# Performance work log

Measured on AMD Instinct MI355X. Metric: run time of the kernel, lower is better.

## Reference

```python
import jax, jax.numpy as jnp
import numpy as np

EMBED = 128
HEADS = 8
HEAD_DIM = EMBED // HEADS


def setup_inputs() -> dict:
    key = jax.random.key(0)
    ks = jax.random.split(key, 11)
    B, T, N, C = 8, 64, 170, EMBED
    s = 1.0 / np.sqrt(C)
    return {
        "values": jax.random.normal(ks[0], (B, T, N, C), dtype=jnp.float32),
        "keys": jax.random.normal(ks[1], (B, T, N, C), dtype=jnp.float32),
        "query": jax.random.normal(ks[2], (B, T, N, C), dtype=jnp.float32),
        "Wv": jax.random.normal(ks[3], (C, C), dtype=jnp.float32) * s,
        "bv": jnp.zeros((C,), dtype=jnp.float32),
        "Wk": jax.random.normal(ks[4], (C, C), dtype=jnp.float32) * s,
        "bk": jnp.zeros((C,), dtype=jnp.float32),
        "Wq": jax.random.normal(ks[5], (C, C), dtype=jnp.float32) * s,
        "bq": jnp.zeros((C,), dtype=jnp.float32),
        "Wo": jax.random.normal(ks[6], (C, C), dtype=jnp.float32) * s,
        "bo": jnp.zeros((C,), dtype=jnp.float32),
    }


def reference(values, keys, query, Wv, bv, Wk, bk, Wq, bq, Wo, bo):
    B, T, N, C = query.shape
    H, D = HEADS, HEAD_DIM
    # Linear projections (torch nn.Linear: x @ W.T + b)
    v = (values @ Wv.T + bv).reshape(B, T, N, H, D)
    k = (keys @ Wk.T + bk).reshape(B, T, N, H, D)
    q = (query @ Wq.T + bq).reshape(B, T, N, H, D)
    # spatial mode: attention over nodes N, independent per (b, t, h)
    energy = jnp.einsum('btqhd,btkhd->btqkh', q, k)  # [B,T,N,N,H]
    scale = jnp.asarray(C, q.dtype) ** 0.5
    attn = jax.nn.softmax(energy / scale, axis=3)
    out = jnp.einsum('btqkh,btkhd->btqhd', attn, v).reshape(B, T, N, H * D)
    return out @ Wo.T + bo
```

## Files before the change

kernel.cpp:

```cpp
#include <hip/hip_runtime.h>
#include <cstdint>

typedef float   f32x4  __attribute__((ext_vector_type(4)));
typedef __bf16  bf16x4 __attribute__((ext_vector_type(4)));
typedef __bf16  bf16x8 __attribute__((ext_vector_type(8)));

#if __has_builtin(__builtin_amdgcn_exp2f)
#define EXP2F(x) __builtin_amdgcn_exp2f(x)
#else
#define EXP2F(x) exp2f(x)
#endif

#define BT_TOTAL 512
#define NNODES 170
#define CDIM 128
#define HEADS 8
#define HDIM 16
#define SLAB (NNODES*HDIM)
#define NPAD 172
#define VSLAB (HDIM*NPAD)
#define QKV_ELEMS ((size_t)BT_TOTAL*HEADS*SLAB)
#define S2L2E 0.12753851f

__global__ __launch_bounds__(512) void qkv_kernel(const float* __restrict__ qin,
    const float* __restrict__ kin, const float* __restrict__ vin,
    const float* __restrict__ Wq, const float* __restrict__ Wk, const float* __restrict__ Wv,
    const float* __restrict__ bq, const float* __restrict__ bk, const float* __restrict__ bv,
    __bf16* __restrict__ qws, __bf16* __restrict__ kws, __bf16* __restrict__ vt) {
    __shared__ __bf16 Wl[128 * 132];
    int t = threadIdx.x;
    int iid = blockIdx.x / BT_TOTAL;
    int bt  = blockIdx.x % BT_TOTAL;
    const float* X    = (iid == 0) ? qin : (iid == 1) ? kin : vin;
    const float* W    = (iid == 0) ? Wq  : (iid == 1) ? Wk  : Wv;
    const float* bias = (iid == 0) ? bq  : (iid == 1) ? bk  : bv;
    float wscale = (iid == 0) ? S2L2E : 1.0f;
    #pragma unroll
    for (int i = 0; i < 8; ++i) {
        int idx = i * 512 + t;
        int r = idx >> 5, c = (idx & 31) * 4;
        f32x4 w4 = *(const f32x4*)&W[r * 128 + c];
        bf16x4 wb = { (__bf16)(w4[0] * wscale), (__bf16)(w4[1] * wscale),
                      (__bf16)(w4[2] * wscale), (__bf16)(w4[3] * wscale) };
        *(bf16x4*)&Wl[r * 132 + c] = wb;
    }
    __syncthreads();

    int w = t >> 6, lane = t & 63, li = lane & 15, l4 = lane >> 4;
    f32x4 zf = {0.f, 0.f, 0.f, 0.f};
    for (int mt = 0; mt < 2; ++mt) {
        int tbase = mt * 128 + w * 16;
        if (tbase >= NNODES) break;
        int mrow = tbase + li;
        bool mvalid = mrow < NNODES;
        const float* xrow = X + ((size_t)(bt * NNODES + mrow)) * CDIM;
        f32x4 acc[8] = {};
        #pragma unroll
        for (int kk = 0; kk < 4; ++kk) {
            int kb = kk * 32 + l4 * 4;
            f32x4 a0 = mvalid ? *(const f32x4*)(xrow + kb)      : zf;
            f32x4 a1 = mvalid ? *(const f32x4*)(xrow + kb + 16) : zf;
            bf16x8 a = { (__bf16)a0[0], (__bf16)a0[1], (__bf16)a0[2], (__bf16)a0[3],
                         (__bf16)a1[0], (__bf16)a1[1], (__bf16)a1[2], (__bf16)a1[3] };
            if (iid < 2) {
                #pragma unroll
                for (int nt = 0; nt < 8; ++nt) {
                    int c = nt * 16 + li;
                    bf16x4 b0 = *(const bf16x4*)&Wl[c * 132 + kb];
                    bf16x4 b1 = *(const bf16x4*)&Wl[c * 132 + kb + 16];
                    bf16x8 b = __builtin_shufflevector(b0, b1, 0, 1, 2, 3, 4, 5, 6, 7);
                    acc[nt] = __builtin_amdgcn_mfma_f32_16x16x32_bf16(b, a, acc[nt], 0, 0, 0);
                }
            } else {
                #pragma unroll
                for (int nt = 0; nt < 8; ++nt) {
                    int c = nt * 16 + li;
                    bf16x4 b0 = *(const bf16x4*)&Wl[c * 132 + kb];
                    bf16x4 b1 = *(const bf16x4*)&Wl[c * 132 + kb + 16];
                    bf16x8 b = __builtin_shufflevector(b0, b1, 0, 1, 2, 3, 4, 5, 6, 7);
                    acc[nt] = __builtin_amdgcn_mfma_f32_16x16x32_bf16(a, b, acc[nt], 0, 0, 0);
                }
            }
        }
        if (iid < 2) {
            __bf16* outb = ((iid == 0) ? qws : kws) + ((size_t)bt * HEADS) * SLAB;
            int n = tbase + li;
            if (n < NNODES) {
                #pragma unroll
                for (int nt = 0; nt < 8; ++nt) {
                    f32x4 b4 = *(const f32x4*)&bias[nt * 16 + l4 * 4];
                    f32x4 o = acc[nt] + b4 * wscale;
                    bf16x4 o4 = { (__bf16)o[0], (__bf16)o[1], (__bf16)o[2], (__bf16)o[3] };
                    *(bf16x4*)&outb[(size_t)nt * SLAB + n * HDIM + l4 * 4] = o4;
                }
            }
        } else {
            __bf16* outb = vt + ((size_t)bt * HEADS) * VSLAB;
            int n0 = tbase + l4 * 4;
            #pragma unroll
            for (int nt = 0; nt < 8; ++nt) {
                int c = nt * 16 + li;
                float bval = bias[c];
                __bf16* dst = outb + (size_t)nt * VSLAB + li * NPAD + n0;
                if (n0 + 3 < NNODES) {
                    bf16x4 o4 = { (__bf16)(acc[nt][0] + bval), (__bf16)(acc[nt][1] + bval),
                                  (__bf16)(acc[nt][2] + bval), (__bf16)(acc[nt][3] + bval) };
                    *(bf16x4*)dst = o4;
                } else {
                    #pragma unroll
                    for (int r = 0; r < 4; ++r)
                        if (n0 + r < NNODES) dst[r] = (__bf16)(acc[nt][r] + bval);
                }
            }
        }
    }
}

__global__ __launch_bounds__(256) void attn_kernel(const __bf16* __restrict__ qws,
                                                   const __bf16* __restrict__ kws,
                                                   const __bf16* __restrict__ vt,
                                                   __bf16* __restrict__ ows) {
    int unit = blockIdx.x * 4 + (threadIdx.x >> 6);
    int half = unit & 1, bh = unit >> 1;
    int bt = bh >> 3, h = bh & 7;
    int lane = threadIdx.x & 63, li = lane & 15, l4 = lane >> 4;
    const __bf16* qb  = qws + ((size_t)(bt * HEADS + h)) * SLAB;
    const __bf16* kb  = kws + ((size_t)(bt * HEADS + h)) * SLAB;
    const __bf16* vtb = vt  + ((size_t)(bt * HEADS + h)) * VSLAB;
    __bf16* ob = ows + (size_t)bt * NNODES * CDIM + h * HDIM;
    const __bf16 bz = (__bf16)0.0f;
    const bf16x4 z4 = {bz, bz, bz, bz};
    const f32x4 zf = {0.f, 0.f, 0.f, 0.f};

    bf16x4 kf[11];
    #pragma unroll
    for (int tt = 0; tt < 11; ++tt)
        kf[tt] = *(const bf16x4*)&kb[(tt * 16 + li) * HDIM + l4 * 4];

    bf16x8 vf[6];
    #pragma unroll
    for (int s = 0; s < 5; ++s) {
        bf16x4 a = *(const bf16x4*)&vtb[li * NPAD + 32 * s + 4 * l4];
        bf16x4 b = *(const bf16x4*)&vtb[li * NPAD + 32 * s + 4 * l4 + 16];
        vf[s] = __builtin_shufflevector(a, b, 0, 1, 2, 3, 4, 5, 6, 7);
    }
    {
        bf16x4 a = *(const bf16x4*)&vtb[li * NPAD + 160 + 4 * l4];
        bf16x8 v5 = { (160 + 4 * l4 + 0 < NNODES) ? a[0] : bz,
                      (160 + 4 * l4 + 1 < NNODES) ? a[1] : bz,
                      (160 + 4 * l4 + 2 < NNODES) ? a[2] : bz,
                      (160 + 4 * l4 + 3 < NNODES) ? a[3] : bz,
                      bz, bz, bz, bz };
        vf[5] = v5;
    }
    f32x4 mk = { (160 + l4 * 4 + 0 < NNODES) ? 1.f : 0.f,
                 (160 + l4 * 4 + 1 < NNODES) ? 1.f : 0.f,
                 (160 + l4 * 4 + 2 < NNODES) ? 1.f : 0.f,
                 (160 + l4 * 4 + 3 < NNODES) ? 1.f : 0.f };

    int q0 = half ? 6 : 0;
    int qn = half ? 5 : 6;
    for (int qi = 0; qi < qn; ++qi) {
        int qc = q0 + qi;
        bf16x4 qv = *(const bf16x4*)&qb[(qc * 16 + li) * HDIM + l4 * 4];
        bf16x8 qf = __builtin_shufflevector(qv, z4, 0, 1, 2, 3, 4, 5, 6, 7);
        bf16x4 ph[11];
        f32x4 s4 = zf;
        #pragma unroll
        for (int tt = 0; tt < 11; ++tt) {
            bf16x8 a = __builtin_shufflevector(kf[tt], z4, 0, 1, 2, 3, 4, 5, 6, 7);
            f32x4 e = __builtin_amdgcn_mfma_f32_16x16x32_bf16(a, qf, zf, 0, 0, 0);
            f32x4 p;
            p[0] = EXP2F(e[0]); p[1] = EXP2F(e[1]);
            p[2] = EXP2F(e[2]); p[3] = EXP2F(e[3]);
            if (tt == 10) p *= mk;
            s4 += p;
            ph[tt] = __builtin_convertvector(p, bf16x4);
        }
        float sum = (s4[0] + s4[1]) + (s4[2] + s4[3]);
        sum += __shfl_xor(sum, 16);
        sum += __shfl_xor(sum, 32);
        float inv = 1.0f / sum;
        f32x4 o0 = zf, o1 = zf;
        o0 = __builtin_amdgcn_mfma_f32_16x16x32_bf16(vf[0],
                __builtin_shufflevector(ph[0], ph[1], 0,1,2,3,4,5,6,7), o0, 0,0,0);
        o1 = __builtin_amdgcn_mfma_f32_16x16x32_bf16(vf[1],
                __builtin_shufflevector(ph[2], ph[3], 0,1,2,3,4,5,6,7), o1, 0,0,0);
        o0 = __builtin_amdgcn_mfma_f32_16x16x32_bf16(vf[2],
                __builtin_shufflevector(ph[4], ph[5], 0,1,2,3,4,5,6,7), o0, 0,0,0);
        o1 = __builtin_amdgcn_mfma_f32_16x16x32_bf16(vf[3],
                __builtin_shufflevector(ph[6], ph[7], 0,1,2,3,4,5,6,7), o1, 0,0,0);
        o0 = __builtin_amdgcn_mfma_f32_16x16x32_bf16(vf[4],
                __builtin_shufflevector(ph[8], ph[9], 0,1,2,3,4,5,6,7), o0, 0,0,0);
        o1 = __builtin_amdgcn_mfma_f32_16x16x32_bf16(vf[5],
                __builtin_shufflevector(ph[10], z4,    0,1,2,3,4,5,6,7), o1, 0,0,0);
        f32x4 o = o0 + o1;
        int q = qc * 16 + li;
        if (q < NNODES) {
            bf16x4 ov = { (__bf16)(o[0] * inv), (__bf16)(o[1] * inv),
                          (__bf16)(o[2] * inv), (__bf16)(o[3] * inv) };
            *(bf16x4*)&ob[(size_t)q * CDIM + l4 * 4] = ov;
        }
    }
}

__global__ __launch_bounds__(512) void oproj_kernel(const __bf16* __restrict__ ows,
                                                    const float* __restrict__ Wo,
                                                    const float* __restrict__ bo,
                                                    float* __restrict__ out) {
    __shared__ __bf16 Wl[128 * 132];
    int t = threadIdx.x;
    int bt = blockIdx.x;
    #pragma unroll
    for (int i = 0; i < 8; ++i) {
        int idx = i * 512 + t;
        int r = idx >> 5, c = (idx & 31) * 4;
        f32x4 w4 = *(const f32x4*)&Wo[r * 128 + c];
        bf16x4 wb = { (__bf16)w4[0], (__bf16)w4[1], (__bf16)w4[2], (__bf16)w4[3] };
        *(bf16x4*)&Wl[r * 132 + c] = wb;
    }
    __syncthreads();

    int w = t >> 6, lane = t & 63, li = lane & 15, l4 = lane >> 4;
    const bf16x4 z4 = {(__bf16)0.f, (__bf16)0.f, (__bf16)0.f, (__bf16)0.f};
    for (int mt = 0; mt < 2; ++mt) {
        int tbase = mt * 128 + w * 16;
        if (tbase >= NNODES) break;
        int mrow = tbase + li;
        bool mvalid = mrow < NNODES;
        const __bf16* arow = ows + ((size_t)bt * NNODES + mrow) * CDIM;
        f32x4 acc[8] = {};
        #pragma unroll
        for (int kk = 0; kk < 4; ++kk) {
            int kb = kk * 32 + l4 * 4;
            bf16x4 a0 = mvalid ? *(const bf16x4*)(arow + kb)      : z4;
            bf16x4 a1 = mvalid ? *(const bf16x4*)(arow + kb + 16) : z4;
            bf16x8 a = __builtin_shufflevector(a0, a1, 0, 1, 2, 3, 4, 5, 6, 7);
            #pragma unroll
            for (int nt = 0; nt < 8; ++nt) {
                int c = nt * 16 + li;
                bf16x4 b0 = *(const bf16x4*)&Wl[c * 132 + kb];
                bf16x4 b1 = *(const bf16x4*)&Wl[c * 132 + kb + 16];
                bf16x8 b = __builtin_shufflevector(b0, b1, 0, 1, 2, 3, 4, 5, 6, 7);
                acc[nt] = __builtin_amdgcn_mfma_f32_16x16x32_bf16(b, a, acc[nt], 0, 0, 0);
            }
        }
        int n = tbase + li;
        if (n < NNODES) {
            float* orow = out + ((size_t)bt * NNODES + n) * CDIM;
            #pragma unroll
            for (int nt = 0; nt < 8; ++nt) {
                f32x4 b4 = *(const f32x4*)&bo[nt * 16 + l4 * 4];
                f32x4 o = acc[nt] + b4;
                *(f32x4*)&orow[nt * 16 + l4 * 4] = o;
            }
        }
    }
}

extern "C" void kernel_launch(void* const* d_in, const int* in_sizes, int n_in,
                              void* d_out, int out_size, void* d_ws, size_t ws_size,
                              hipStream_t stream) {
    const float* values = (const float*)d_in[0];
    const float* keys   = (const float*)d_in[1];
    const float* query  = (const float*)d_in[2];
    const float* Wv = (const float*)d_in[3];
    const float* bv = (const float*)d_in[4];
    const float* Wk = (const float*)d_in[5];
    const float* bk = (const float*)d_in[6];
    const float* Wq = (const float*)d_in[7];
    const float* bq = (const float*)d_in[8];
    const float* Wo = (const float*)d_in[9];
    const float* bo = (const float*)d_in[10];
    float* out = (float*)d_out;

    __bf16* qws = (__bf16*)d_ws;
    __bf16* kws = qws + QKV_ELEMS;
    __bf16* ows = kws + QKV_ELEMS;
    __bf16* vt  = (__bf16*)d_out;

    hipLaunchKernelGGL(qkv_kernel,  dim3(1536), dim3(512), 0, stream,
                       query, keys, values, Wq, Wk, Wv, bq, bk, bv, qws, kws, vt);
    hipLaunchKernelGGL(attn_kernel, dim3(2048), dim3(256), 0, stream, qws, kws, vt, ows);
    hipLaunchKernelGGL(oproj_kernel, dim3(512), dim3(512), 0, stream, ows, Wo, bo, out);
}
```

Baseline: 102.2 us.

## Fuse QKV projection, attention and output projection into one per-timestep kernel

Merges the three kernels into one block per (b,t). The block computes Q, K and V into shared memory, runs attention for all 8 heads (one wave per head), stages the head outputs in shared memory and applies the output projection there. A small pre-kernel converts all four weight matrices to bf16 in MFMA fragment order so waves can load them straight into registers. This removes the global round-trips for Q/K/V/O intermediates and two launches. In exchange it uses 128KB of shared memory per block, so only 512 blocks run at low occupancy, and each wave holds 32 weight fragments in registers.

```diff
diff --git a/kernel.cpp b/kernel.cpp
--- a/kernel.cpp
+++ b/kernel.cpp
@@ -16,243 +16,227 @@
 #define CDIM 128
 #define HEADS 8
 #define HDIM 16
-#define SLAB (NNODES*HDIM)
 #define NPAD 172
-#define VSLAB (HDIM*NPAD)
-#define QKV_ELEMS ((size_t)BT_TOTAL*HEADS*SLAB)
 #define S2L2E 0.12753851f
 
-__global__ __launch_bounds__(512) void qkv_kernel(const float* __restrict__ qin,
+#define QOFF 0
+#define KOFF 21760
+#define VOFF 43520
+#define OSTRIDE 132
+#define SMEM_ELEMS 65536
+
+__global__ __launch_bounds__(256) void wconv_kernel(const float* __restrict__ wq,
+                                                    const float* __restrict__ wk,
+                                                    const float* __restrict__ wv,
+                                                    const float* __restrict__ wo,
+                                                    __bf16* __restrict__ wbf) {
+    int idx = blockIdx.x * 256 + threadIdx.x;
+    if (idx >= 4 * 16384) return;
+    int mat = idx >> 14, rem = idx & 16383;
+    int c = rem >> 7, o = rem & 127;
+    int kk = o >> 5, l4 = (o & 31) >> 3, j = o & 7;
+    int col = kk * 32 + l4 * 4 + (j & 3) + 16 * (j >> 2);
+    const float* W = (mat == 0) ? wq : (mat == 1) ? wk : (mat == 2) ? wv : wo;
+    float scale = (mat == 0) ? S2L2E : 1.0f;
+    wbf[idx] = (__bf16)(W[c * 128 + col] * scale);
+}
+
+__global__ __launch_bounds__(512, 2) void fused_kernel(const float* __restrict__ qin,
     const float* __restrict__ kin, const float* __restrict__ vin,
-    const float* __restrict__ Wq, const float* __restrict__ Wk, const float* __restrict__ Wv,
-    const float* __restrict__ bq, const float* __restrict__ bk, const float* __restrict__ bv,
-    __bf16* __restrict__ qws, __bf16* __restrict__ kws, __bf16* __restrict__ vt) {
-    __shared__ __bf16 Wl[128 * 132];
-    int t = threadIdx.x;
-    int iid = blockIdx.x / BT_TOTAL;
-    int bt  = blockIdx.x % BT_TOTAL;
-    const float* X    = (iid == 0) ? qin : (iid == 1) ? kin : vin;
-    const float* W    = (iid == 0) ? Wq  : (iid == 1) ? Wk  : Wv;
-    const float* bias = (iid == 0) ? bq  : (iid == 1) ? bk  : bv;
-    float wscale = (iid == 0) ? S2L2E : 1.0f;
-    #pragma unroll
-    for (int i = 0; i < 8; ++i) {
-        int idx = i * 512 + t;
-        int r = idx >> 5, c = (idx & 31) * 4;
-        f32x4 w4 = *(const f32x4*)&W[r * 128 + c];
-        bf16x4 wb = { (__bf16)(w4[0] * wscale), (__bf16)(w4[1] * wscale),
-                      (__bf16)(w4[2] * wscale), (__bf16)(w4[3] * wscale) };
-        *(bf16x4*)&Wl[r * 132 + c] = wb;
-    }
-    __syncthreads();
-
-    int w = t >> 6, lane = t & 63, li = lane & 15, l4 = lane >> 4;
-    f32x4 zf = {0.f, 0.f, 0.f, 0.f};
-    for (int mt = 0; mt < 2; ++mt) {
-        int tbase = mt * 128 + w * 16;
-        if (tbase >= NNODES) break;
-        int mrow = tbase + li;
-        bool mvalid = mrow < NNODES;
-        const float* xrow = X + ((size_t)(bt * NNODES + mrow)) * CDIM;
-        f32x4 acc[8] = {};
-        #pragma unroll
-        for (int kk = 0; kk < 4; ++kk) {
-            int kb = kk * 32 + l4 * 4;
-            f32x4 a0 = mvalid ? *(const f32x4*)(xrow + kb)      : zf;
-            f32x4 a1 = mvalid ? *(const f32x4*)(xrow + kb + 16) : zf;
-            bf16x8 a = { (__bf16)a0[0], (__bf16)a0[1], (__bf16)a0[2], (__bf16)a0[3],
-                         (__bf16)a1[0], (__bf16)a1[1], (__bf16)a1[2], (__bf16)a1[3] };
-            if (iid < 2) {
-                #pragma unroll
-                for (int nt = 0; nt < 8; ++nt) {
-                    int c = nt * 16 + li;
-                    bf16x4 b0 = *(const bf16x4*)&Wl[c * 132 + kb];
-                    bf16x4 b1 = *(const bf16x4*)&Wl[c * 132 + kb + 16];
-                    bf16x8 b = __builtin_shufflevector(b0, b1, 0, 1, 2, 3, 4, 5, 6, 7);
-                    acc[nt] = __builtin_amdgcn_mfma_f32_16x16x32_bf16(b, a, acc[nt], 0, 0, 0);
-                }
-            } else {
-                #pragma unroll
-                for (int nt = 0; nt < 8; ++nt) {
-                    int c = nt * 16 + li;
-                    bf16x4 b0 = *(const bf16x4*)&Wl[c * 132 + kb];
-                    bf16x4 b1 = *(const bf16x4*)&Wl[c * 132 + kb + 16];
-                    bf16x8 b = __builtin_shufflevector(b0, b1, 0, 1, 2, 3, 4, 5, 6, 7);
-                    acc[nt] = __builtin_amdgcn_mfma_f32_16x16x32_bf16(a, b, acc[nt], 0, 0, 0);
-                }
-            }
-        }
-        if (iid < 2) {
-            __bf16* outb = ((iid == 0) ? qws : kws) + ((size_t)bt * HEADS) * SLAB;
-            int n = tbase + li;
-            if (n < NNODES) {
-                #pragma unroll
-                for (int nt = 0; nt < 8; ++nt) {
-                    f32x4 b4 = *(const f32x4*)&bias[nt * 16 + l4 * 4];
-                    f32x4 o = acc[nt] + b4 * wscale;
-                    bf16x4 o4 = { (__bf16)o[0], (__bf16)o[1], (__bf16)o[2], (__bf16)o[3] };
-                    *(bf16x4*)&outb[(size_t)nt * SLAB + n * HDIM + l4 * 4] = o4;
-                }
-            }
-        } else {
-            __bf16* outb = vt + ((size_t)bt * HEADS) * VSLAB;
-            int n0 = tbase + l4 * 4;
-            #pragma unroll
-            for (int nt = 0; nt < 8; ++nt) {
-                int c = nt * 16 + li;
-                float bval = bias[c];
-                __bf16* dst = outb + (size_t)nt * VSLAB + li * NPAD + n0;
-                if (n0 + 3 < NNODES) {
-                    bf16x4 o4 = { (__bf16)(acc[nt][0] + bval), (__bf16)(acc[nt][1] + bval),
-                                  (__bf16)(acc[nt][2] + bval), (__bf16)(acc[nt][3] + bval) };
-                    *(bf16x4*)dst = o4;
-                } else {
-                    #pragma unroll
-                    for (int r = 0; r < 4; ++r)
-                        if (n0 + r < NNODES) dst[r] = (__bf16)(acc[nt][r] + bval);
-                }
-            }
-        }
-    }
-}
-
-__global__ __launch_bounds__(256) void attn_kernel(const __bf16* __restrict__ qws,
-                                                   const __bf16* __restrict__ kws,
-                                                   const __bf16* __restrict__ vt,
-                                                   __bf16* __restrict__ ows) {
-    int unit = blockIdx.x * 4 + (threadIdx.x >> 6);
-    int half = unit & 1, bh = unit >> 1;
-    int bt = bh >> 3, h = bh & 7;
-    int lane = threadIdx.x & 63, li = lane & 15, l4 = lane >> 4;
-    const __bf16* qb  = qws + ((size_t)(bt * HEADS + h)) * SLAB;
-    const __bf16* kb  = kws + ((size_t)(bt * HEADS + h)) * SLAB;
-    const __bf16* vtb = vt  + ((size_t)(bt * HEADS + h)) * VSLAB;
-    __bf16* ob = ows + (size_t)bt * NNODES * CDIM + h * HDIM;
+    const __bf16* __restrict__ wbf,
+    const float* __restrict__ bq, const float* __restrict__ bk,
+    const float* __restrict__ bv, const float* __restrict__ bo,
+    float* __restrict__ out) {
+    __shared__ __align__(16) __bf16 smem[SMEM_ELEMS];
+    __bf16* qL = smem + QOFF;
+    __bf16* kL = smem + KOFF;
+    __bf16* vL = smem + VOFF;
+    __bf16* oL = smem;
+
+    int bt = blockIdx.x;
+    int t = threadIdx.x, w = t >> 6, lane = t & 63, li = lane & 15, l4 = lane >> 4;
     const __bf16 bz = (__bf16)0.0f;
     const bf16x4 z4 = {bz, bz, bz, bz};
     const f32x4 zf = {0.f, 0.f, 0.f, 0.f};
 
-    bf16x4 kf[11];
+    {
+        int iid = (w < 3) ? 0 : (w < 6 ? 1 : 2);
+        int g   = w - ((iid == 0) ? 0 : (iid == 1) ? 3 : 6);
+        int nw  = (iid == 2) ? 2 : 3;
+        const float* X    = (iid == 0) ? qin : (iid == 1) ? kin : vin;
+        const float* bias = (iid == 0) ? bq  : (iid == 1) ? bk  : bv;
+        float wscale = (iid == 0) ? S2L2E : 1.0f;
+        const __bf16* wb = wbf + iid * 16384;
+        bf16x8 bf[8][4];
+        #pragma unroll
+        for (int nt = 0; nt < 8; ++nt)
+            #pragma unroll
+            for (int kk = 0; kk < 4; ++kk)
+                bf[nt][kk] = *(const bf16x8*)&wb[(nt * 16 + li) * 128 + kk * 32 + l4 * 8];
+
+        for (int tile = g; tile < 11; tile += nw) {
+            int tbase = tile * 16;
+            int mrow = tbase + li;
+            bool mvalid = mrow < NNODES;
+            const float* xrow = X + ((size_t)(bt * NNODES + mrow)) * CDIM;
+            f32x4 acc[8] = {};
+            #pragma unroll
+            for (int kk = 0; kk < 4; ++kk) {
+                int kb = kk * 32 + l4 * 4;
+                f32x4 a0 = mvalid ? *(const f32x4*)(xrow + kb)      : zf;
+                f32x4 a1 = mvalid ? *(const f32x4*)(xrow + kb + 16) : zf;
+                bf16x8 a = { (__bf16)a0[0], (__bf16)a0[1], (__bf16)a0[2], (__bf16)a0[3],
+                             (__bf16)a1[0], (__bf16)a1[1], (__bf16)a1[2], (__bf16)a1[3] };
+                if (iid < 2) {
+                    #pragma unroll
+                    for (int nt = 0; nt < 8; ++nt)
+                        acc[nt] = __builtin_amdgcn_mfma_f32_16x16x32_bf16(bf[nt][kk], a, acc[nt], 0, 0, 0);
+                } else {
+                    #pragma unroll
+                    for (int nt = 0; nt < 8; ++nt)
+                        acc[nt] = __builtin_amdgcn_mfma_f32_16x16x32_bf16(a, bf[nt][kk], acc[nt], 0, 0, 0);
+                }
+            }
+            if (iid < 2) {
+                __bf16* dst = (iid == 0) ? qL : kL;
+                int n = tbase + li;
+                if (n < NNODES) {
+                    #pragma unroll
+                    for (int nt = 0; nt < 8; ++nt) {
+                        f32x4 b4 = *(const f32x4*)&bias[nt * 16 + l4 * 4];
+                        f32x4 ov = acc[nt] + b4 * wscale;
+                        bf16x4 o4 = { (__bf16)ov[0], (__bf16)ov[1], (__bf16)ov[2], (__bf16)ov[3] };
+                        *(bf16x4*)&dst[nt * (NNODES * HDIM) + n * HDIM + l4 * 4] = o4;
+                    }
+                }
+            } else {
+                int n0 = tbase + l4 * 4;
+                #pragma unroll
+                for (int nt = 0; nt < 8; ++nt) {
+                    float bval = bias[nt * 16 + li];
+                    __bf16* d2 = vL + nt * (HDIM * NPAD) + li * NPAD + n0;
+                    if (n0 + 3 < NNODES) {
+                        bf16x4 o4 = { (__bf16)(acc[nt][0] + bval), (__bf16)(acc[nt][1] + bval),
+                                      (__bf16)(acc[nt][2] + bval), (__bf16)(acc[nt][3] + bval) };
+                        *(bf16x4*)d2 = o4;
+                    } else {
+                        #pragma unroll
+                        for (int r = 0; r < 4; ++r)
+                            if (n0 + r < NNODES) d2[r] = (__bf16)(acc[nt][r] + bval);
+                    }
+                }
+            }
+        }
+    }
+    __syncthreads();
+
+    bf16x4 obf[11];
+    {
+        const __bf16* qh = qL + w * (NNODES * HDIM);
+        const __bf16* kh = kL + w * (NNODES * HDIM);
+        const __bf16* vh = vL + w * (HDIM * NPAD);
+        bf16x4 kf[11];
+        #pragma unroll
+        for (int tt = 0; tt < 11; ++tt)
+            kf[tt] = *(const bf16x4*)&kh[(tt * 16 + li) * HDIM + l4 * 4];
+        bf16x8 vf[6];
+        #pragma unroll
+        for (int s = 0; s < 5; ++s) {
+            bf16x4 a = *(const bf16x4*)&vh[li * NPAD + 32 * s + 4 * l4];
+            bf16x4 b = *(const bf16x4*)&vh[li * NPAD + 32 * s + 4 * l4 + 16];
+            vf[s] = __builtin_shufflevector(a, b, 0, 1, 2, 3, 4, 5, 6, 7);
+        }
+        {
+            bf16x4 a = *(const bf16x4*)&vh[li * NPAD + 160 + 4 * l4];
+            bf16x8 v5 = { (160 + 4 * l4 + 0 < NNODES) ? a[0] : bz,
+                          (160 + 4 * l4 + 1 < NNODES) ? a[1] : bz,
+                          (160 + 4 * l4 + 2 < NNODES) ? a[2] : bz,
+                          (160 + 4 * l4 + 3 < NNODES) ? a[3] : bz,
+                          bz, bz, bz, bz };
+            vf[5] = v5;
+        }
+        for (int qc = 0; qc < 11; ++qc) {
+            bf16x4 qv = *(const bf16x4*)&qh[(qc * 16 + li) * HDIM + l4 * 4];
+            bf16x8 qf = __builtin_shufflevector(qv, z4, 0, 1, 2, 3, 4, 5, 6, 7);
+            bf16x4 ph[11];
+            f32x4 s4 = zf;
+            #pragma unroll
+            for (int tt = 0; tt < 11; ++tt) {
+                bf16x8 a = __builtin_shufflevector(kf[tt], z4, 0, 1, 2, 3, 4, 5, 6, 7);
+                f32x4 e = __builtin_amdgcn_mfma_f32_16x16x32_bf16(a, qf, zf, 0, 0, 0);
+                if (tt == 10) {
+                    #pragma unroll
+                    for (int r = 0; r < 4; ++r)
+                        e[r] = (160 + l4 * 4 + r < NNODES) ? e[r] : -1.0e30f;
+                }
+                f32x4 p;
+                p[0] = EXP2F(e[0]); p[1] = EXP2F(e[1]);
+                p[2] = EXP2F(e[2]); p[3] = EXP2F(e[3]);
+                s4 += p;
+                ph[tt] = __builtin_convertvector(p, bf16x4);
+            }
+            float sum = (s4[0] + s4[1]) + (s4[2] + s4[3]);
+            sum += __shfl_xor(sum, 16);
+            sum += __shfl_xor(sum, 32);
+            float inv = 1.0f / sum;
+            f32x4 o0 = zf, o1 = zf;
+            o0 = __builtin_amdgcn_mfma_f32_16x16x32_bf16(vf[0],
+                    __builtin_shufflevector(ph[0], ph[1], 0,1,2,3,4,5,6,7), o0, 0,0,0);
+            o1 = __builtin_amdgcn_mfma_f32_16x16x32_bf16(vf[1],
+                    __builtin_shufflevector(ph[2], ph[3], 0,1,2,3,4,5,6,7), o1, 0,0,0);
+            o0 = __builtin_amdgcn_mfma_f32_16x16x32_bf16(vf[2],
+                    __builtin_shufflevector(ph[4], ph[5], 0,1,2,3,4,5,6,7), o0, 0,0,0);
+            o1 = __builtin_amdgcn_mfma_f32_16x16x32_bf16(vf[3],
+                    __builtin_shufflevector(ph[6], ph[7], 0,1,2,3,4,5,6,7), o1, 0,0,0);
+            o0 = __builtin_amdgcn_mfma_f32_16x16x32_bf16(vf[4],
+                    __builtin_shufflevector(ph[8], ph[9], 0,1,2,3,4,5,6,7), o0, 0,0,0);
+            o1 = __builtin_amdgcn_mfma_f32_16x16x32_bf16(vf[5],
+                    __builtin_shufflevector(ph[10], z4,    0,1,2,3,4,5,6,7), o1, 0,0,0);
+            f32x4 o = (o0 + o1) * inv;
+            obf[qc] = (bf16x4){ (__bf16)o[0], (__bf16)o[1], (__bf16)o[2], (__bf16)o[3] };
+        }
+    }
+    __syncthreads();
+
     #pragma unroll
-    for (int tt = 0; tt < 11; ++tt)
-        kf[tt] = *(const bf16x4*)&kb[(tt * 16 + li) * HDIM + l4 * 4];
-
-    bf16x8 vf[6];
-    #pragma unroll
-    for (int s = 0; s < 5; ++s) {
-        bf16x4 a = *(const bf16x4*)&vtb[li * NPAD + 32 * s + 4 * l4];
-        bf16x4 b = *(const bf16x4*)&vtb[li * NPAD + 32 * s + 4 * l4 + 16];
-        vf[s] = __builtin_shufflevector(a, b, 0, 1, 2, 3, 4, 5, 6, 7);
-    }
+    for (int qc = 0; qc < 11; ++qc) {
+        int q = qc * 16 + li;
+        if (q < NNODES)
+            *(bf16x4*)&oL[(size_t)q * OSTRIDE + w * HDIM + l4 * 4] = obf[qc];
+    }
+    __syncthreads();
+
     {
-        bf16x4 a = *(const bf16x4*)&vtb[li * NPAD + 160 + 4 * l4];
-        bf16x8 v5 = { (160 + 4 * l4 + 0 < NNODES) ? a[0] : bz,
-                      (160 + 4 * l4 + 1 < NNODES) ? a[1] : bz,
-                      (160 + 4 * l4 + 2 < NNODES) ? a[2] : bz,
-                      (160 + 4 * l4 + 3 < NNODES) ? a[3] : bz,
-                      bz, bz, bz, bz };
-        vf[5] = v5;
-    }
-    f32x4 mk = { (160 + l4 * 4 + 0 < NNODES) ? 1.f : 0.f,
-                 (160 + l4 * 4 + 1 < NNODES) ? 1.f : 0.f,
-                 (160 + l4 * 4 + 2 < NNODES) ? 1.f : 0.f,
-                 (160 + l4 * 4 + 3 < NNODES) ? 1.f : 0.f };
-
-    int q0 = half ? 6 : 0;
-    int qn = half ? 5 : 6;
-    for (int qi = 0; qi < qn; ++qi) {
-        int qc = q0 + qi;
-        bf16x4 qv = *(const bf16x4*)&qb[(qc * 16 + li) * HDIM + l4 * 4];
-        bf16x8 qf = __builtin_shufflevector(qv, z4, 0, 1, 2, 3, 4, 5, 6, 7);
-        bf16x4 ph[11];
-        f32x4 s4 = zf;
-        #pragma unroll
-        for (int tt = 0; tt < 11; ++tt) {
-            bf16x8 a = __builtin_shufflevector(kf[tt], z4, 0, 1, 2, 3, 4, 5, 6, 7);
-            f32x4 e = __builtin_amdgcn_mfma_f32_16x16x32_bf16(a, qf, zf, 0, 0, 0);
-            f32x4 p;
-            p[0] = EXP2F(e[0]); p[1] = EXP2F(e[1]);
-            p[2] = EXP2F(e[2]); p[3] = EXP2F(e[3]);
-            if (tt == 10) p *= mk;
-            s4 += p;
-            ph[tt] = __builtin_convertvector(p, bf16x4);
-        }
-        float sum = (s4[0] + s4[1]) + (s4[2] + s4[3]);
-        sum += __shfl_xor(sum, 16);
-        sum += __shfl_xor(sum, 32);
-        float inv = 1.0f / sum;
-        f32x4 o0 = zf, o1 = zf;
-        o0 = __builtin_amdgcn_mfma_f32_16x16x32_bf16(vf[0],
-                __builtin_shufflevector(ph[0], ph[1], 0,1,2,3,4,5,6,7), o0, 0,0,0);
-        o1 = __builtin_amdgcn_mfma_f32_16x16x32_bf16(vf[1],
-                __builtin_shufflevector(ph[2], ph[3], 0,1,2,3,4,5,6,7), o1, 0,0,0);
-        o0 = __builtin_amdgcn_mfma_f32_16x16x32_bf16(vf[2],
-                __builtin_shufflevector(ph[4], ph[5], 0,1,2,3,4,5,6,7), o0, 0,0,0);
-        o1 = __builtin_amdgcn_mfma_f32_16x16x32_bf16(vf[3],
-                __builtin_shufflevector(ph[6], ph[7], 0,1,2,3,4,5,6,7), o1, 0,0,0);
-        o0 = __builtin_amdgcn_mfma_f32_16x16x32_bf16(vf[4],
-                __builtin_shufflevector(ph[8], ph[9], 0,1,2,3,4,5,6,7), o0, 0,0,0);
-        o1 = __builtin_amdgcn_mfma_f32_16x16x32_bf16(vf[5],
-                __builtin_shufflevector(ph[10], z4,    0,1,2,3,4,5,6,7), o1, 0,0,0);
-        f32x4 o = o0 + o1;
-        int q = qc * 16 + li;
-        if (q < NNODES) {
-            bf16x4 ov = { (__bf16)(o[0] * inv), (__bf16)(o[1] * inv),
-                          (__bf16)(o[2] * inv), (__bf16)(o[3] * inv) };
-            *(bf16x4*)&ob[(size_t)q * CDIM + l4 * 4] = ov;
-        }
-    }
-}
-
-__global__ __launch_bounds__(512) void oproj_kernel(const __bf16* __restrict__ ows,
-                                                    const float* __restrict__ Wo,
-                                                    const float* __restrict__ bo,
-                                                    float* __restrict__ out) {
-    __shared__ __bf16 Wl[128 * 132];
-    int t = threadIdx.x;
-    int bt = blockIdx.x;
-    #pragma unroll
-    for (int i = 0; i < 8; ++i) {
-        int idx = i * 512 + t;
-        int r = idx >> 5, c = (idx & 31) * 4;
-        f32x4 w4 = *(const f32x4*)&Wo[r * 128 + c];
-        bf16x4 wb = { (__bf16)w4[0], (__bf16)w4[1], (__bf16)w4[2], (__bf16)w4[3] };
-        *(bf16x4*)&Wl[r * 132 + c] = wb;
-    }
-    __syncthreads();
-
-    int w = t >> 6, lane = t & 63, li = lane & 15, l4 = lane >> 4;
-    const bf16x4 z4 = {(__bf16)0.f, (__bf16)0.f, (__bf16)0.f, (__bf16)0.f};
-    for (int mt = 0; mt < 2; ++mt) {
-        int tbase = mt * 128 + w * 16;
-        if (tbase >= NNODES) break;
-        int mrow = tbase + li;
-        bool mvalid = mrow < NNODES;
-        const __bf16* arow = ows + ((size_t)bt * NNODES + mrow) * CDIM;
-        f32x4 acc[8] = {};
-        #pragma unroll
-        for (int kk = 0; kk < 4; ++kk) {
-            int kb = kk * 32 + l4 * 4;
-            bf16x4 a0 = mvalid ? *(const bf16x4*)(arow + kb)      : z4;
-            bf16x4 a1 = mvalid ? *(const bf16x4*)(arow + kb + 16) : z4;
-            bf16x8 a = __builtin_shufflevector(a0, a1, 0, 1, 2, 3, 4, 5, 6, 7);
-            #pragma unroll
-            for (int nt = 0; nt < 8; ++nt) {
-                int c = nt * 16 + li;
-                bf16x4 b0 = *(const bf16x4*)&Wl[c * 132 + kb];
-                bf16x4 b1 = *(const bf16x4*)&Wl[c * 132 + kb + 16];
-                bf16x8 b = __builtin_shufflevector(b0, b1, 0, 1, 2, 3, 4, 5, 6, 7);
-                acc[nt] = __builtin_amdgcn_mfma_f32_16x16x32_bf16(b, a, acc[nt], 0, 0, 0);
-            }
-        }
-        int n = tbase + li;
-        if (n < NNODES) {
-            float* orow = out + ((size_t)bt * NNODES + n) * CDIM;
-            #pragma unroll
-            for (int nt = 0; nt < 8; ++nt) {
-                f32x4 b4 = *(const f32x4*)&bo[nt * 16 + l4 * 4];
-                f32x4 o = acc[nt] + b4;
-                *(f32x4*)&orow[nt * 16 + l4 * 4] = o;
+        const __bf16* wo = wbf + 3 * 16384;
+        bf16x8 of[8][4];
+        #pragma unroll
+        for (int nt = 0; nt < 8; ++nt)
+            #pragma unroll
+            for (int kk = 0; kk < 4; ++kk)
+                of[nt][kk] = *(const bf16x8*)&wo[(nt * 16 + li) * 128 + kk * 32 + l4 * 8];
+
+        for (int tile = w; tile < 11; tile += 8) {
+            int tbase = tile * 16;
+            int mrow = tbase + li;
+            f32x4 acc[8] = {};
+            #pragma unroll
+            for (int kk = 0; kk < 4; ++kk) {
+                int kb = kk * 32 + l4 * 4;
+                bf16x4 a0 = *(const bf16x4*)&oL[(size_t)mrow * OSTRIDE + kb];
+                bf16x4 a1 = *(const bf16x4*)&oL[(size_t)mrow * OSTRIDE + kb + 16];
+                bf16x8 a = __builtin_shufflevector(a0, a1, 0, 1, 2, 3, 4, 5, 6, 7);
+                #pragma unroll
+                for (int nt = 0; nt < 8; ++nt)
+                    acc[nt] = __builtin_amdgcn_mfma_f32_16x16x32_bf16(of[nt][kk], a, acc[nt], 0, 0, 0);
+            }
+            int n = tbase + li;
+            if (n < NNODES) {
+                float* orow = out + ((size_t)bt * NNODES + n) * CDIM;
+                #pragma unroll
+                for (int nt = 0; nt < 8; ++nt) {
+                    f32x4 b4 = *(const f32x4*)&bo[nt * 16 + l4 * 4];
+                    *(f32x4*)&orow[nt * 16 + l4 * 4] = acc[nt] + b4;
+                }
             }
         }
     }
@@ -273,14 +257,9 @@
     const float* Wo = (const float*)d_in[9];
     const float* bo = (const float*)d_in[10];
     float* out = (float*)d_out;
-
-    __bf16* qws = (__bf16*)d_ws;
-    __bf16* kws = qws + QKV_ELEMS;
-    __bf16* ows = kws + QKV_ELEMS;
-    __bf16* vt  = (__bf16*)d_out;
-
-    hipLaunchKernelGGL(qkv_kernel,  dim3(1536), dim3(512), 0, stream,
-                       query, keys, values, Wq, Wk, Wv, bq, bk, bv, qws, kws, vt);
-    hipLaunchKernelGGL(attn_kernel, dim3(2048), dim3(256), 0, stream, qws, kws, vt, ows);
-    hipLaunchKernelGGL(oproj_kernel, dim3(512), dim3(512), 0, stream, ows, Wo, bo, out);
+    __bf16* wbf = (__bf16*)d_ws;
+
+    hipLaunchKernelGGL(wconv_kernel, dim3(256), dim3(256), 0, stream, Wq, Wk, Wv, Wo, wbf);
+    hipLaunchKernelGGL(fused_kernel, dim3(BT_TOTAL), dim3(512), 0, stream,
+                       query, keys, values, wbf, bq, bk, bv, bo, out);
 }
```

New measurement: 111.0 us. 1.09x slower.

## Pre-convert weights to permuted bf16, pipeline A loads, permute ows layout

Applied to the files above, without the earlier changes.

Adds a small kernel that converts and permutes all four weight matrices to bf16 once per call, so the projection kernels load weights with contiguous 16-byte reads instead of converting fp32 per block. The qkv kernel moves to 256-thread blocks and software-pipelines the activation tile loads across three tiles per wave. The attention output is written in a permuted column order so oproj can read 8 contiguous bf16 per lane. Tail masking now sets padded logits to a large negative value before exp, and NPAD grows to 176. The cost is an extra kernel launch and more workspace.

```diff
diff --git a/kernel.cpp b/kernel.cpp
--- a/kernel.cpp
+++ b/kernel.cpp
@@ -17,103 +17,117 @@
 #define HEADS 8
 #define HDIM 16
 #define SLAB (NNODES*HDIM)
-#define NPAD 172
+#define NPAD 176
 #define VSLAB (HDIM*NPAD)
 #define QKV_ELEMS ((size_t)BT_TOTAL*HEADS*SLAB)
+#define WPAD 136
 #define S2L2E 0.12753851f
 
-__global__ __launch_bounds__(512) void qkv_kernel(const float* __restrict__ qin,
+__global__ __launch_bounds__(256) void wconv_kernel(const float* __restrict__ wq,
+                                                    const float* __restrict__ wk,
+                                                    const float* __restrict__ wv,
+                                                    const float* __restrict__ wo,
+                                                    __bf16* __restrict__ wbf) {
+    int idx = blockIdx.x * 256 + threadIdx.x;
+    if (idx >= 4 * 16384) return;
+    int mat = idx >> 14, rem = idx & 16383;
+    int c = rem >> 7, o = rem & 127;
+    int kk = o >> 5, l4 = (o & 31) >> 3, j = o & 7;
+    int col = kk * 32 + l4 * 4 + (j & 3) + 16 * (j >> 2);
+    const float* W = (mat == 0) ? wq : (mat == 1) ? wk : (mat == 2) ? wv : wo;
+    float scale = (mat == 0) ? S2L2E : 1.0f;
+    wbf[idx] = (__bf16)(W[c * 128 + col] * scale);
+}
+
+__global__ __launch_bounds__(256, 4) void qkv_kernel(const float* __restrict__ qin,
     const float* __restrict__ kin, const float* __restrict__ vin,
-    const float* __restrict__ Wq, const float* __restrict__ Wk, const float* __restrict__ Wv,
+    const __bf16* __restrict__ wbf,
     const float* __restrict__ bq, const float* __restrict__ bk, const float* __restrict__ bv,
     __bf16* __restrict__ qws, __bf16* __restrict__ kws, __bf16* __restrict__ vt) {
-    __shared__ __bf16 Wl[128 * 132];
+    __shared__ __bf16 Wl[128 * WPAD];
     int t = threadIdx.x;
     int iid = blockIdx.x / BT_TOTAL;
     int bt  = blockIdx.x % BT_TOTAL;
     const float* X    = (iid == 0) ? qin : (iid == 1) ? kin : vin;
-    const float* W    = (iid == 0) ? Wq  : (iid == 1) ? Wk  : Wv;
     const float* bias = (iid == 0) ? bq  : (iid == 1) ? bk  : bv;
     float wscale = (iid == 0) ? S2L2E : 1.0f;
+    const __bf16* wb = wbf + iid * 16384;
     #pragma unroll
     for (int i = 0; i < 8; ++i) {
-        int idx = i * 512 + t;
-        int r = idx >> 5, c = (idx & 31) * 4;
-        f32x4 w4 = *(const f32x4*)&W[r * 128 + c];
-        bf16x4 wb = { (__bf16)(w4[0] * wscale), (__bf16)(w4[1] * wscale),
-                      (__bf16)(w4[2] * wscale), (__bf16)(w4[3] * wscale) };
-        *(bf16x4*)&Wl[r * 132 + c] = wb;
+        int idx = i * 256 + t;
+        int c = idx >> 4, x = (idx & 15) * 8;
+        *(bf16x8*)&Wl[c * WPAD + x] = *(const bf16x8*)&wb[idx * 8];
     }
     __syncthreads();
 
     int w = t >> 6, lane = t & 63, li = lane & 15, l4 = lane >> 4;
-    f32x4 zf = {0.f, 0.f, 0.f, 0.f};
-    for (int mt = 0; mt < 2; ++mt) {
-        int tbase = mt * 128 + w * 16;
-        if (tbase >= NNODES) break;
-        int mrow = tbase + li;
-        bool mvalid = mrow < NNODES;
-        const float* xrow = X + ((size_t)(bt * NNODES + mrow)) * CDIM;
+    const f32x4 zf = {0.f, 0.f, 0.f, 0.f};
+
+    auto loadA = [&](f32x4* A, int tile) {
+        int mrow = tile * 16 + li;
+        bool v = mrow < NNODES;
+        const float* xr = X + ((size_t)(bt * NNODES + mrow)) * CDIM;
+        #pragma unroll
+        for (int kk = 0; kk < 4; ++kk) {
+            A[2 * kk]     = v ? *(const f32x4*)(xr + kk * 32 + l4 * 4)      : zf;
+            A[2 * kk + 1] = v ? *(const f32x4*)(xr + kk * 32 + l4 * 4 + 16) : zf;
+        }
+    };
+    auto compute = [&](const f32x4* A, int tile) {
         f32x4 acc[8] = {};
         #pragma unroll
         for (int kk = 0; kk < 4; ++kk) {
-            int kb = kk * 32 + l4 * 4;
-            f32x4 a0 = mvalid ? *(const f32x4*)(xrow + kb)      : zf;
-            f32x4 a1 = mvalid ? *(const f32x4*)(xrow + kb + 16) : zf;
+            f32x4 a0 = A[2 * kk], a1 = A[2 * kk + 1];
             bf16x8 a = { (__bf16)a0[0], (__bf16)a0[1], (__bf16)a0[2], (__bf16)a0[3],
                          (__bf16)a1[0], (__bf16)a1[1], (__bf16)a1[2], (__bf16)a1[3] };
-            if (iid < 2) {
-                #pragma unroll
-                for (int nt = 0; nt < 8; ++nt) {
-                    int c = nt * 16 + li;
-                    bf16x4 b0 = *(const bf16x4*)&Wl[c * 132 + kb];
-                    bf16x4 b1 = *(const bf16x4*)&Wl[c * 132 + kb + 16];
-                    bf16x8 b = __builtin_shufflevector(b0, b1, 0, 1, 2, 3, 4, 5, 6, 7);
+            #pragma unroll
+            for (int nt = 0; nt < 8; ++nt) {
+                bf16x8 b = *(const bf16x8*)&Wl[(nt * 16 + li) * WPAD + kk * 32 + l4 * 8];
+                if (iid < 2)
                     acc[nt] = __builtin_amdgcn_mfma_f32_16x16x32_bf16(b, a, acc[nt], 0, 0, 0);
-                }
-            } else {
-                #pragma unroll
-                for (int nt = 0; nt < 8; ++nt) {
-                    int c = nt * 16 + li;
-                    bf16x4 b0 = *(const bf16x4*)&Wl[c * 132 + kb];
-                    bf16x4 b1 = *(const bf16x4*)&Wl[c * 132 + kb + 16];
-                    bf16x8 b = __builtin_shufflevector(b0, b1, 0, 1, 2, 3, 4, 5, 6, 7);
+                else
                     acc[nt] = __builtin_amdgcn_mfma_f32_16x16x32_bf16(a, b, acc[nt], 0, 0, 0);
-                }
             }
         }
         if (iid < 2) {
-            __bf16* outb = ((iid == 0) ? qws : kws) + ((size_t)bt * HEADS) * SLAB;
-            int n = tbase + li;
+            __bf16* dst = ((iid == 0) ? qws : kws) + (size_t)bt * HEADS * SLAB;
+            int n = tile * 16 + li;
             if (n < NNODES) {
                 #pragma unroll
                 for (int nt = 0; nt < 8; ++nt) {
                     f32x4 b4 = *(const f32x4*)&bias[nt * 16 + l4 * 4];
-                    f32x4 o = acc[nt] + b4 * wscale;
-                    bf16x4 o4 = { (__bf16)o[0], (__bf16)o[1], (__bf16)o[2], (__bf16)o[3] };
-                    *(bf16x4*)&outb[(size_t)nt * SLAB + n * HDIM + l4 * 4] = o4;
+                    f32x4 ov = acc[nt] + b4 * wscale;
+                    bf16x4 o4 = { (__bf16)ov[0], (__bf16)ov[1], (__bf16)ov[2], (__bf16)ov[3] };
+                    *(bf16x4*)&dst[(size_t)nt * SLAB + n * HDIM + l4 * 4] = o4;
                 }
             }
         } else {
-            __bf16* outb = vt + ((size_t)bt * HEADS) * VSLAB;
-            int n0 = tbase + l4 * 4;
+            __bf16* dst = vt + (size_t)bt * HEADS * VSLAB;
+            int n0 = tile * 16 + l4 * 4;
             #pragma unroll
             for (int nt = 0; nt < 8; ++nt) {
-                int c = nt * 16 + li;
-                float bval = bias[c];
-                __bf16* dst = outb + (size_t)nt * VSLAB + li * NPAD + n0;
+                float bval = bias[nt * 16 + li];
+                __bf16* d2 = dst + (size_t)nt * VSLAB + li * NPAD + n0;
                 if (n0 + 3 < NNODES) {
                     bf16x4 o4 = { (__bf16)(acc[nt][0] + bval), (__bf16)(acc[nt][1] + bval),
                                   (__bf16)(acc[nt][2] + bval), (__bf16)(acc[nt][3] + bval) };
-                    *(bf16x4*)dst = o4;
+                    *(bf16x4*)d2 = o4;
                 } else {
                     #pragma unroll
                     for (int r = 0; r < 4; ++r)
-                        if (n0 + r < NNODES) dst[r] = (__bf16)(acc[nt][r] + bval);
+                        if (n0 + r < NNODES) d2[r] = (__bf16)(acc[nt][r] + bval);
                 }
             }
         }
-    }
+    };
+
+    f32x4 A0[8], A1[8];
+    loadA(A0, w);
+    loadA(A1, w + 4);
+    compute(A0, w);
+    if (w < 3) loadA(A0, w + 8);
+    compute(A1, w + 4);
+    if (w < 3) compute(A0, w + 8);
 }
 
 __global__ __launch_bounds__(256) void attn_kernel(const __bf16* __restrict__ qws,
@@ -127,7 +141,7 @@
     const __bf16* qb  = qws + ((size_t)(bt * HEADS + h)) * SLAB;
     const __bf16* kb  = kws + ((size_t)(bt * HEADS + h)) * SLAB;
     const __bf16* vtb = vt  + ((size_t)(bt * HEADS + h)) * VSLAB;
-    __bf16* ob = ows + (size_t)bt * NNODES * CDIM + h * HDIM;
+    __bf16* ob = ows + (size_t)bt * NNODES * CDIM + (h >> 1) * 32 + (h & 1) * 4;
     const __bf16 bz = (__bf16)0.0f;
     const bf16x4 z4 = {bz, bz, bz, bz};
     const f32x4 zf = {0.f, 0.f, 0.f, 0.f};
@@ -153,10 +167,6 @@
                       bz, bz, bz, bz };
         vf[5] = v5;
     }
-    f32x4 mk = { (160 + l4 * 4 + 0 < NNODES) ? 1.f : 0.f,
-                 (160 + l4 * 4 + 1 < NNODES) ? 1.f : 0.f,
-                 (160 + l4 * 4 + 2 < NNODES) ? 1.f : 0.f,
-                 (160 + l4 * 4 + 3 < NNODES) ? 1.f : 0.f };
 
     int q0 = half ? 6 : 0;
     int qn = half ? 5 : 6;
@@ -170,10 +180,14 @@
         for (int tt = 0; tt < 11; ++tt) {
             bf16x8 a = __builtin_shufflevector(kf[tt], z4, 0, 1, 2, 3, 4, 5, 6, 7);
             f32x4 e = __builtin_amdgcn_mfma_f32_16x16x32_bf16(a, qf, zf, 0, 0, 0);
+            if (tt == 10) {
+                #pragma unroll
+                for (int r = 0; r < 4; ++r)
+                    e[r] = (160 + l4 * 4 + r < NNODES) ? e[r] : -1.0e30f;
+            }
             f32x4 p;
             p[0] = EXP2F(e[0]); p[1] = EXP2F(e[1]);
             p[2] = EXP2F(e[2]); p[3] = EXP2F(e[3]);
-            if (tt == 10) p *= mk;
             s4 += p;
             ph[tt] = __builtin_convertvector(p, bf16x4);
         }
@@ -194,68 +208,68 @@
                 __builtin_shufflevector(ph[8], ph[9], 0,1,2,3,4,5,6,7), o0, 0,0,0);
         o1 = __builtin_amdgcn_mfma_f32_16x16x32_bf16(vf[5],
                 __builtin_shufflevector(ph[10], z4,    0,1,2,3,4,5,6,7), o1, 0,0,0);
-        f32x4 o = o0 + o1;
+        f32x4 o = (o0 + o1) * inv;
         int q = qc * 16 + li;
         if (q < NNODES) {
-            bf16x4 ov = { (__bf16)(o[0] * inv), (__bf16)(o[1] * inv),
-                          (__bf16)(o[2] * inv), (__bf16)(o[3] * inv) };
-            *(bf16x4*)&ob[(size_t)q * CDIM + l4 * 4] = ov;
+            bf16x4 ov = { (__bf16)o[0], (__bf16)o[1], (__bf16)o[2], (__bf16)o[3] };
+            *(bf16x4*)&ob[(size_t)q * CDIM + l4 * 8] = ov;
         }
     }
 }
 
 __global__ __launch_bounds__(512) void oproj_kernel(const __bf16* __restrict__ ows,
-                                                    const float* __restrict__ Wo,
+                                                    const __bf16* __restrict__ wbf,
                                                     const float* __restrict__ bo,
                                                     float* __restrict__ out) {
-    __shared__ __bf16 Wl[128 * 132];
+    __shared__ __bf16 Wl[128 * WPAD];
     int t = threadIdx.x;
     int bt = blockIdx.x;
+    const __bf16* wo = wbf + 3 * 16384;
     #pragma unroll
-    for (int i = 0; i < 8; ++i) {
+    for (int i = 0; i < 4; ++i) {
         int idx = i * 512 + t;
-        int r = idx >> 5, c = (idx & 31) * 4;
-        f32x4 w4 = *(const f32x4*)&Wo[r * 128 + c];
-        bf16x4 wb = { (__bf16)w4[0], (__bf16)w4[1], (__bf16)w4[2], (__bf16)w4[3] };
-        *(bf16x4*)&Wl[r * 132 + c] = wb;
+        int c = idx >> 4, x = (idx & 15) * 8;
+        *(bf16x8*)&Wl[c * WPAD + x] = *(const bf16x8*)&wo[idx * 8];
     }
     __syncthreads();
 
     int w = t >> 6, lane = t & 63, li = lane & 15, l4 = lane >> 4;
-    const bf16x4 z4 = {(__bf16)0.f, (__bf16)0.f, (__bf16)0.f, (__bf16)0.f};
-    for (int mt = 0; mt < 2; ++mt) {
-        int tbase = mt * 128 + w * 16;
-        if (tbase >= NNODES) break;
-        int mrow = tbase + li;
-        bool mvalid = mrow < NNODES;
-        const __bf16* arow = ows + ((size_t)bt * NNODES + mrow) * CDIM;
+    const bf16x8 z8 = {};
+
+    auto loadO = [&](bf16x8* A, int tile) {
+        int mrow = tile * 16 + li;
+        bool v = mrow < NNODES;
+        const __bf16* ar = ows + ((size_t)(bt * NNODES + mrow)) * CDIM;
+        #pragma unroll
+        for (int kk = 0; kk < 4; ++kk)
+            A[kk] = v ? *(const bf16x8*)(ar + kk * 32 + l4 * 8) : z8;
+    };
+    auto computeO = [&](const bf16x8* A, int tile) {
         f32x4 acc[8] = {};
         #pragma unroll
         for (int kk = 0; kk < 4; ++kk) {
-            int kb = kk * 32 + l4 * 4;
-            bf16x4 a0 = mvalid ? *(const bf16x4*)(arow + kb)      : z4;
-            bf16x4 a1 = mvalid ? *(const bf16x4*)(arow + kb + 16) : z4;
-            bf16x8 a = __builtin_shufflevector(a0, a1, 0, 1, 2, 3, 4, 5, 6, 7);
             #pragma unroll
             for (int nt = 0; nt < 8; ++nt) {
-                int c = nt * 16 + li;
-                bf16x4 b0 = *(const bf16x4*)&Wl[c * 132 + kb];
-                bf16x4 b1 = *(const bf16x4*)&Wl[c * 132 + kb + 16];
-                bf16x8 b = __builtin_shufflevector(b0, b1, 0, 1, 2, 3, 4, 5, 6, 7);
-                acc[nt] = __builtin_amdgcn_mfma_f32_16x16x32_bf16(b, a, acc[nt], 0, 0, 0);
-            }
-        }
-        int n = tbase + li;
+                bf16x8 b = *(const bf16x8*)&Wl[(nt * 16 + li) * WPAD + kk * 32 + l4 * 8];
+                acc[nt] = __builtin_amdgcn_mfma_f32_16x16x32_bf16(b, A[kk], acc[nt], 0, 0, 0);
+            }
+        }
+        int n = tile * 16 + li;
         if (n < NNODES) {
             float* orow = out + ((size_t)bt * NNODES + n) * CDIM;
             #pragma unroll
             for (int nt = 0; nt < 8; ++nt) {
                 f32x4 b4 = *(const f32x4*)&bo[nt * 16 + l4 * 4];
-                f32x4 o = acc[nt] + b4;
-                *(f32x4*)&orow[nt * 16 + l4 * 4] = o;
-            }
-        }
-    }
+                *(f32x4*)&orow[nt * 16 + l4 * 4] = acc[nt] + b4;
+            }
+        }
+    };
+
+    bf16x8 A0[4], A1[4];
+    loadO(A0, w);
+    if (w < 3) loadO(A1, w + 8);
+    computeO(A0, w);
+    if (w < 3) computeO(A1, w + 8);
 }
 
 extern "C" void kernel_launch(void* const* d_in, const int* in_sizes, int n_in,
@@ -277,10 +291,12 @@
     __bf16* qws = (__bf16*)d_ws;
     __bf16* kws = qws + QKV_ELEMS;
     __bf16* ows = kws + QKV_ELEMS;
+    __bf16* wbf = ows + QKV_ELEMS;
     __bf16* vt  = (__bf16*)d_out;
 
-    hipLaunchKernelGGL(qkv_kernel,  dim3(1536), dim3(512), 0, stream,
-                       query, keys, values, Wq, Wk, Wv, bq, bk, bv, qws, kws, vt);
-    hipLaunchKernelGGL(attn_kernel, dim3(2048), dim3(256), 0, stream, qws, kws, vt, ows);
-    hipLaunchKernelGGL(oproj_kernel, dim3(512), dim3(512), 0, stream, ows, Wo, bo, out);
-}
+    hipLaunchKernelGGL(wconv_kernel, dim3(256),  dim3(256), 0, stream, Wq, Wk, Wv, Wo, wbf);
+    hipLaunchKernelGGL(qkv_kernel,   dim3(1536), dim3(256), 0, stream,
+                       query, keys, values, wbf, bq, bk, bv, qws, kws, vt);
+    hipLaunchKernelGGL(attn_kernel,  dim3(2048), dim3(256), 0, stream, qws, kws, vt, ows);
+    hipLaunchKernelGGL(oproj_kernel, dim3(512),  dim3(512), 0, stream, ows, wbf, bo, out);
+}
```

Result: no change. 103.5 us (+1.3%).
